# Performance work log

Hardware: AMD Instinct MI355X
Metric: run time of the kernel (lower is better)

Reference implementation:

```python
import jax, jax.numpy as jnp
import numpy as np

D_MODEL = 1024
N_HEAD = 16
D_K = D_MODEL // N_HEAD
SEQ_LEN = 2048
BATCH = 2
NEG = -1e8


def setup_inputs() -> dict:
    key = jax.random.key(0)
    ks = jax.random.split(key, 8)
    scale = 1.0 / np.sqrt(D_MODEL)
    inp = {
        "input": jax.random.normal(ks[0], (BATCH, SEQ_LEN, D_MODEL), dtype=jnp.float32),
        "mask": jax.random.randint(ks[1], (BATCH, SEQ_LEN), 0, 2) == 1,  # True = masked
        "Wq": jax.random.uniform(ks[2], (D_MODEL, D_MODEL), jnp.float32, -scale, scale),
        "bq": jax.random.uniform(ks[3], (D_MODEL,), jnp.float32, -scale, scale),
        "Wk": jax.random.uniform(ks[4], (D_MODEL, D_MODEL), jnp.float32, -scale, scale),
        "bk": jax.random.uniform(ks[5], (D_MODEL,), jnp.float32, -scale, scale),
        "Wv": jax.random.uniform(ks[6], (D_MODEL, D_MODEL), jnp.float32, -scale, scale),
        "bv": jax.random.uniform(ks[7], (D_MODEL,), jnp.float32, -scale, scale),
    }
    return inp


def reference(input, mask, Wq, bq, Wk, bk, Wv, bv):
    B, S, D = input.shape
    # nn.Linear: y = x @ W^T + b
    def split_heads(x):
        return x.reshape(B, S, N_HEAD, D_K).transpose(0, 2, 1, 3)  # [B,H,S,d_k]

    Q = split_heads(input @ Wq.T + bq)
    K = split_heads(input @ Wk.T + bk)
    V = split_heads(input @ Wv.T + bv)

    scores = jnp.einsum('bhqd,bhkd->bhqk', Q, K) / jnp.sqrt(jnp.float32(D_K))
    # mask [B,S] broadcast over heads and query positions (key mask)
    scores = jnp.where(mask[:, None, None, :], NEG, scores)
    attn = jax.nn.softmax(scores, axis=-1)
    out = jnp.einsum('bhqk,bhkd->bhqd', attn, V)  # [B,H,S,d_k]
    return out.transpose(0, 2, 1, 3).reshape(B, S, D)
```

## Files before the change

### kernel.cpp

```cpp
#include <hip/hip_runtime.h>
#include <math.h>

#define D_MODEL 1024
#define NH 16
#define DK 64
#define SEQ 2048
#define BATCH 2
#define MTOT (BATCH * SEQ)

typedef unsigned short u16;
typedef unsigned int u32;
typedef short bf16x8 __attribute__((ext_vector_type(8)));
typedef short bf16x4 __attribute__((ext_vector_type(4)));
typedef float f32x4 __attribute__((ext_vector_type(4)));

static constexpr float NEGV2 = -1e8f * 1.44269504089f;
static constexpr float SCL2  = 0.125f * 1.44269504089f;
static constexpr float MINIT = -1e30f;

__device__ __forceinline__ u16 f2bf(float f) {
    union { float f; u32 u; } v; v.f = f;
    u32 r = v.u + 0x7FFFu + ((v.u >> 16) & 1u);
    return (u16)(r >> 16);
}

__device__ __forceinline__ float fexp2(float x) {
#if __has_builtin(__builtin_amdgcn_exp2f)
    return __builtin_amdgcn_exp2f(x);
#else
    return __expf(x * 0.69314718056f);
#endif
}

__device__ __forceinline__ f32x4 mfma16(bf16x4 a, bf16x4 b, f32x4 c) {
#if __has_builtin(__builtin_amdgcn_mfma_f32_16x16x16_bf16)
    return __builtin_amdgcn_mfma_f32_16x16x16_bf16(a, b, c, 0, 0, 0);
#else
    return __builtin_amdgcn_mfma_f32_16x16x16bf16_1k(a, b, c, 0, 0, 0);
#endif
}

__device__ __forceinline__ void stage16(const u16* g, u16* lds_per_lane) {
#if __has_builtin(__builtin_amdgcn_global_load_lds)
    __builtin_amdgcn_global_load_lds((const __attribute__((address_space(1))) u32*)g,
                                     (__attribute__((address_space(3))) u32*)lds_per_lane,
                                     16, 0, 0);
#else
    *(uint4*)lds_per_lane = *(const uint4*)g;
#endif
}

__global__ __launch_bounds__(256) void convert_bf16(
    const float* __restrict__ X, const float* __restrict__ Wq,
    const float* __restrict__ Wk, const float* __restrict__ Wv,
    u16* __restrict__ Xb, u16* __restrict__ Wb)
{
    const int NX = MTOT * D_MODEL / 4;
    const int NW = D_MODEL * D_MODEL / 4;
    int i = blockIdx.x * 256 + threadIdx.x;
    if (i >= NX + 3 * NW) return;
    float4 v; u16* dst;
    if (i < NX)             { v = ((const float4*)X )[i];            dst = Xb + (size_t)i * 4; }
    else if (i < NX + NW)   { v = ((const float4*)Wq)[i - NX];       dst = Wb + (size_t)(i - NX) * 4; }
    else if (i < NX + 2*NW) { v = ((const float4*)Wk)[i - NX - NW];  dst = Wb + (size_t)NW * 4 + (size_t)(i - NX - NW) * 4; }
    else                    { v = ((const float4*)Wv)[i - NX - 2*NW];dst = Wb + (size_t)NW * 8 + (size_t)(i - NX - 2*NW) * 4; }
    ushort4 o;
    o.x = f2bf(v.x); o.y = f2bf(v.y); o.z = f2bf(v.z); o.w = f2bf(v.w);
    *(ushort4*)dst = o;
}

__global__ __launch_bounds__(256, 2) void proj_mfma(
    const u16* __restrict__ Xb, const u16* __restrict__ Wb,
    const float* __restrict__ bq, const float* __restrict__ bk, const float* __restrict__ bv,
    u16* __restrict__ Qb, u16* __restrict__ Kb, u16* __restrict__ Vb)
{
    __shared__ u16 As[128 * 32];
    __shared__ u16 Bs[128 * 32];

    const int which = blockIdx.z;
    const u16* __restrict__ W = Wb + (size_t)which * D_MODEL * D_MODEL;
    const float* __restrict__ bias = which == 0 ? bq : (which == 1 ? bk : bv);
    u16* __restrict__ Out = which == 0 ? Qb : (which == 1 ? Kb : Vb);

    const int m0 = blockIdx.x * 128, n0 = blockIdx.y * 128;
    const int tid = threadIdx.x, lane = tid & 63, w = tid >> 6;
    const int quad = lane >> 4, l15 = lane & 15;
    const int wr = w >> 1, wc = w & 1;

    f32x4 acc[4][4];
#pragma unroll
    for (int i = 0; i < 4; i++)
#pragma unroll
        for (int j = 0; j < 4; j++) acc[i][j] = (f32x4)0.0f;

    const int srow = 32 * w + (lane >> 2);
    const int scol = (lane & 3) * 8;

    for (int k0 = 0; k0 < D_MODEL; k0 += 32) {
#pragma unroll
        for (int t = 0; t < 2; t++) {
            stage16(Xb + (size_t)(m0 + srow + 16 * t) * D_MODEL + k0 + scol,
                    &As[(32 * w + 16 * t) * 32 + lane * 8]);
            stage16(W + (size_t)(n0 + srow + 16 * t) * D_MODEL + k0 + scol,
                    &Bs[(32 * w + 16 * t) * 32 + lane * 8]);
        }
        __syncthreads();
        bf16x8 af[4], bfr[4];
#pragma unroll
        for (int i = 0; i < 4; i++)
            af[i] = *(const bf16x8*)&As[(wr * 64 + i * 16 + l15) * 32 + quad * 8];
#pragma unroll
        for (int j = 0; j < 4; j++)
            bfr[j] = *(const bf16x8*)&Bs[(wc * 64 + j * 16 + l15) * 32 + quad * 8];
#pragma unroll
        for (int i = 0; i < 4; i++)
#pragma unroll
            for (int j = 0; j < 4; j++)
                acc[i][j] = __builtin_amdgcn_mfma_f32_16x16x32_bf16(af[i], bfr[j], acc[i][j], 0, 0, 0);
        __syncthreads();
    }

    float bj[4];
#pragma unroll
    for (int j = 0; j < 4; j++) bj[j] = bias[n0 + wc * 64 + j * 16 + l15];
#pragma unroll
    for (int i = 0; i < 4; i++) {
#pragma unroll
        for (int j = 0; j < 4; j++) {
#pragma unroll
            for (int r = 0; r < 4; r++) {
                int m = m0 + wr * 64 + i * 16 + quad * 4 + r;
                int n = n0 + wc * 64 + j * 16 + l15;
                int b = m >> 11, s = m & (SEQ - 1);
                int h = n >> 6, d = n & 63;
                Out[(((size_t)b * NH + h) * SEQ + s) * DK + d] = f2bf(acc[i][j][r] + bj[j]);
            }
        }
    }
}

__global__ __launch_bounds__(256, 2) void attn_mfma(
    const u16* __restrict__ Qg, const u16* __restrict__ Kg, const u16* __restrict__ Vg,
    const int* __restrict__ mask, float* __restrict__ out)
{
    constexpr int PADK = 72, PADV = 72;
    __shared__ u16 Ks[2][64 * PADK];
    __shared__ u16 Vt[2][64 * PADV];
    __shared__ float mads[SEQ];

    const int qt0 = blockIdx.x, h = blockIdx.y, b = blockIdx.z;
    const int tid = threadIdx.x, lane = tid & 63, w = tid >> 6;
    const int quad = lane >> 4, l15 = lane & 15;
    const size_t bh = (size_t)b * NH + h;
    const u16* __restrict__ Qp = Qg + (bh * SEQ + qt0 * 128) * DK;
    const u16* __restrict__ Kp = Kg + bh * SEQ * DK;
    const u16* __restrict__ Vp = Vg + bh * SEQ * DK;
    const int* __restrict__ mp = mask + b * SEQ;

    for (int i = tid; i < SEQ; i += 256) mads[i] = mp[i] ? NEGV2 : 0.0f;

    const int q0 = w * 32;
    bf16x8 qf[2][2];
#pragma unroll
    for (int qt = 0; qt < 2; qt++)
#pragma unroll
        for (int half = 0; half < 2; half++)
            qf[qt][half] = *(const bf16x8*)(Qp + (size_t)(q0 + qt * 16 + l15) * DK + half * 32 + quad * 8);

    const int skey = tid & 63, sdk = (tid >> 6) * 16;
    const int vkp2 = (tid & 31) * 2, vd0 = (tid >> 5) * 8;

    {
        const u16* kr = Kp + (size_t)skey * DK + sdk;
        bf16x8 k0 = *(const bf16x8*)kr, k1 = *(const bf16x8*)(kr + 8);
        u16* kd = &Ks[0][skey * PADK + sdk];
        *(bf16x8*)kd = k0; *(bf16x8*)(kd + 8) = k1;
        const u16* vr = Vp + (size_t)vkp2 * DK + vd0;
        bf16x8 v0 = *(const bf16x8*)vr, v1 = *(const bf16x8*)(vr + DK);
#pragma unroll
        for (int i = 0; i < 8; i++)
            *(u32*)&Vt[0][(vd0 + i) * PADV + vkp2] = (u32)(u16)v0[i] | ((u32)(u16)v1[i] << 16);
    }
    __syncthreads();

    f32x4 O[4][2];
    float mrow[2], lrow[2];
#pragma unroll
    for (int dt = 0; dt < 4; dt++)
#pragma unroll
        for (int qt = 0; qt < 2; qt++) O[dt][qt] = (f32x4)0.0f;
    mrow[0] = mrow[1] = MINIT;
    lrow[0] = lrow[1] = 0.0f;

    for (int kt = 0; kt < SEQ / 64; kt++) {
        const int bb = kt & 1;
        bf16x8 nk0, nk1, nv0, nv1;
        if (kt < SEQ / 64 - 1) {
            const u16* kr = Kp + (size_t)((kt + 1) * 64 + skey) * DK + sdk;
            nk0 = *(const bf16x8*)kr; nk1 = *(const bf16x8*)(kr + 8);
            const u16* vr = Vp + (size_t)((kt + 1) * 64 + vkp2) * DK + vd0;
            nv0 = *(const bf16x8*)vr; nv1 = *(const bf16x8*)(vr + DK);
        }

        f32x4 St[4][2];
#pragma unroll
        for (int ktl = 0; ktl < 4; ktl++) {
            bf16x8 kf0 = *(const bf16x8*)&Ks[bb][(ktl * 16 + l15) * PADK + quad * 8];
            bf16x8 kf1 = *(const bf16x8*)&Ks[bb][(ktl * 16 + l15) * PADK + 32 + quad * 8];
#pragma unroll
            for (int qt = 0; qt < 2; qt++) {
                f32x4 acc = (f32x4)0.0f;
                acc = __builtin_amdgcn_mfma_f32_16x16x32_bf16(kf0, qf[qt][0], acc, 0, 0, 0);
                acc = __builtin_amdgcn_mfma_f32_16x16x32_bf16(kf1, qf[qt][1], acc, 0, 0, 0);
                St[ktl][qt] = acc;
            }
        }

#pragma unroll
        for (int ktl = 0; ktl < 4; ktl++) {
            f32x4 ma = *(const f32x4*)&mads[kt * 64 + ktl * 16 + quad * 4];
#pragma unroll
            for (int qt = 0; qt < 2; qt++)
#pragma unroll
                for (int r = 0; r < 4; r++)
                    St[ktl][qt][r] = St[ktl][qt][r] * SCL2 + ma[r];
        }

        float alpha[2];
#pragma unroll
        for (int qt = 0; qt < 2; qt++) {
            float mx = St[0][qt][0];
#pragma unroll
            for (int ktl = 0; ktl < 4; ktl++)
#pragma unroll
                for (int r = 0; r < 4; r++) mx = fmaxf(mx, St[ktl][qt][r]);
            mx = fmaxf(mx, __shfl_xor(mx, 16));
            mx = fmaxf(mx, __shfl_xor(mx, 32));
            float mn = fmaxf(mrow[qt], mx);
            alpha[qt] = fexp2(mrow[qt] - mn);
            mrow[qt] = mn;
            float sum = 0.0f;
#pragma unroll
            for (int ktl = 0; ktl < 4; ktl++)
#pragma unroll
                for (int r = 0; r < 4; r++) {
                    float p = fexp2(St[ktl][qt][r] - mn);
                    St[ktl][qt][r] = p;
                    sum += p;
                }
            sum += __shfl_xor(sum, 16);
            sum += __shfl_xor(sum, 32);
            lrow[qt] = alpha[qt] * lrow[qt] + sum;
        }

        bf16x4 pf[4][2];
#pragma unroll
        for (int ktl = 0; ktl < 4; ktl++)
#pragma unroll
            for (int qt = 0; qt < 2; qt++) {
                bf16x4 pp;
#pragma unroll
                for (int r = 0; r < 4; r++) pp[r] = (short)f2bf(St[ktl][qt][r]);
                pf[ktl][qt] = pp;
            }

#pragma unroll
        for (int dt = 0; dt < 4; dt++)
#pragma unroll
            for (int qt = 0; qt < 2; qt++)
#pragma unroll
                for (int r = 0; r < 4; r++) O[dt][qt][r] *= alpha[qt];

#pragma unroll
        for (int ktl = 0; ktl < 4; ktl++)
#pragma unroll
            for (int dt = 0; dt < 4; dt++) {
                bf16x4 vf = *(const bf16x4*)&Vt[bb][(dt * 16 + l15) * PADV + ktl * 16 + quad * 4];
#pragma unroll
                for (int qt = 0; qt < 2; qt++)
                    O[dt][qt] = mfma16(vf, pf[ktl][qt], O[dt][qt]);
            }

        if (kt < SEQ / 64 - 1) {
            u16* kd = &Ks[bb ^ 1][skey * PADK + sdk];
            *(bf16x8*)kd = nk0; *(bf16x8*)(kd + 8) = nk1;
#pragma unroll
            for (int i = 0; i < 8; i++)
                *(u32*)&Vt[bb ^ 1][(vd0 + i) * PADV + vkp2] = (u32)(u16)nv0[i] | ((u32)(u16)nv1[i] << 16);
        }
        __syncthreads();
    }

    float inv[2] = {1.0f / lrow[0], 1.0f / lrow[1]};
#pragma unroll
    for (int qt = 0; qt < 2; qt++) {
        int q = qt0 * 128 + q0 + qt * 16 + l15;
        float* op = out + ((size_t)b * SEQ + q) * D_MODEL + h * DK;
#pragma unroll
        for (int dt = 0; dt < 4; dt++)
#pragma unroll
            for (int r = 0; r < 4; r++)
                op[dt * 16 + quad * 4 + r] = O[dt][qt][r] * inv[qt];
    }
}

extern "C" void kernel_launch(void* const* d_in, const int* in_sizes, int n_in,
                              void* d_out, int out_size, void* d_ws, size_t ws_size,
                              hipStream_t stream)
{
    const float* X  = (const float*)d_in[0];
    const int* mask = (const int*)d_in[1];
    const float* Wq = (const float*)d_in[2];
    const float* bq = (const float*)d_in[3];
    const float* Wk = (const float*)d_in[4];
    const float* bk = (const float*)d_in[5];
    const float* Wv = (const float*)d_in[6];
    const float* bv = (const float*)d_in[7];
    float* out = (float*)d_out;

    u16* Xb = (u16*)d_ws;
    u16* Wb = Xb + (size_t)MTOT * D_MODEL;
    u16* Qb = Wb + (size_t)3 * D_MODEL * D_MODEL;
    u16* Kb = Qb + (size_t)BATCH * NH * SEQ * DK;
    u16* Vb = Kb + (size_t)BATCH * NH * SEQ * DK;

    const int ncvt = (MTOT * D_MODEL + 3 * D_MODEL * D_MODEL) / 4;
    convert_bf16<<<(ncvt + 255) / 256, 256, 0, stream>>>(X, Wq, Wk, Wv, Xb, Wb);
    proj_mfma<<<dim3(MTOT / 128, D_MODEL / 128, 3), 256, 0, stream>>>(Xb, Wb, bq, bk, bv, Qb, Kb, Vb);
    attn_mfma<<<dim3(SEQ / 128, NH, BATCH), 256, 0, stream>>>(Qb, Kb, Vb, mask, out);
}
```

Measured before the change: 187.0 us.

## Split attention block into 8 waves of 16 query rows each

The attention kernel now runs 512 threads per block. Each wave owns 16 query rows instead of 32, and the cooperative K/V tile loads are split across more threads. The aim is more waves in flight to hide LDS and exp latency, and lower register pressure per thread. In exchange, each K/V fragment read from shared memory feeds half as many MFMAs, so LDS traffic per FLOP doubles, and barriers now synchronize more waves.

```diff
diff --git a/kernel.cpp b/kernel.cpp
--- a/kernel.cpp
+++ b/kernel.cpp
@@ -139,7 +139,7 @@
     }
 }
 
-__global__ __launch_bounds__(256, 2) void attn_mfma(
+__global__ __launch_bounds__(512, 4) void attn_mfma(
     const u16* __restrict__ Qg, const u16* __restrict__ Kg, const u16* __restrict__ Vg,
     const int* __restrict__ mask, float* __restrict__ out)
 {
@@ -157,150 +157,123 @@
     const u16* __restrict__ Vp = Vg + bh * SEQ * DK;
     const int* __restrict__ mp = mask + b * SEQ;
 
-    for (int i = tid; i < SEQ; i += 256) mads[i] = mp[i] ? NEGV2 : 0.0f;
-
-    const int q0 = w * 32;
-    bf16x8 qf[2][2];
-#pragma unroll
-    for (int qt = 0; qt < 2; qt++)
-#pragma unroll
-        for (int half = 0; half < 2; half++)
-            qf[qt][half] = *(const bf16x8*)(Qp + (size_t)(q0 + qt * 16 + l15) * DK + half * 32 + quad * 8);
-
-    const int skey = tid & 63, sdk = (tid >> 6) * 16;
-    const int vkp2 = (tid & 31) * 2, vd0 = (tid >> 5) * 8;
+    for (int i = tid; i < SEQ; i += 512) mads[i] = mp[i] ? NEGV2 : 0.0f;
+
+    const int q0 = w * 16;
+    bf16x8 qf[2];
+#pragma unroll
+    for (int half = 0; half < 2; half++)
+        qf[half] = *(const bf16x8*)(Qp + (size_t)(q0 + l15) * DK + half * 32 + quad * 8);
+
+    const int skey = tid & 63, sdk = (tid >> 6) * 8;
+    const int vkp2 = (tid & 31) * 2, vd0 = (tid >> 5) * 4;
 
     {
-        const u16* kr = Kp + (size_t)skey * DK + sdk;
-        bf16x8 k0 = *(const bf16x8*)kr, k1 = *(const bf16x8*)(kr + 8);
-        u16* kd = &Ks[0][skey * PADK + sdk];
-        *(bf16x8*)kd = k0; *(bf16x8*)(kd + 8) = k1;
+        *(bf16x8*)&Ks[0][skey * PADK + sdk] = *(const bf16x8*)(Kp + (size_t)skey * DK + sdk);
         const u16* vr = Vp + (size_t)vkp2 * DK + vd0;
-        bf16x8 v0 = *(const bf16x8*)vr, v1 = *(const bf16x8*)(vr + DK);
-#pragma unroll
-        for (int i = 0; i < 8; i++)
+        bf16x4 v0 = *(const bf16x4*)vr, v1 = *(const bf16x4*)(vr + DK);
+#pragma unroll
+        for (int i = 0; i < 4; i++)
             *(u32*)&Vt[0][(vd0 + i) * PADV + vkp2] = (u32)(u16)v0[i] | ((u32)(u16)v1[i] << 16);
     }
     __syncthreads();
 
-    f32x4 O[4][2];
-    float mrow[2], lrow[2];
-#pragma unroll
-    for (int dt = 0; dt < 4; dt++)
-#pragma unroll
-        for (int qt = 0; qt < 2; qt++) O[dt][qt] = (f32x4)0.0f;
-    mrow[0] = mrow[1] = MINIT;
-    lrow[0] = lrow[1] = 0.0f;
+    f32x4 O[4];
+    float mrow = MINIT, lrow = 0.0f;
+#pragma unroll
+    for (int dt = 0; dt < 4; dt++) O[dt] = (f32x4)0.0f;
 
     for (int kt = 0; kt < SEQ / 64; kt++) {
         const int bb = kt & 1;
-        bf16x8 nk0, nk1, nv0, nv1;
+        bf16x8 nk; bf16x4 nv0, nv1;
         if (kt < SEQ / 64 - 1) {
-            const u16* kr = Kp + (size_t)((kt + 1) * 64 + skey) * DK + sdk;
-            nk0 = *(const bf16x8*)kr; nk1 = *(const bf16x8*)(kr + 8);
+            nk = *(const bf16x8*)(Kp + (size_t)((kt + 1) * 64 + skey) * DK + sdk);
             const u16* vr = Vp + (size_t)((kt + 1) * 64 + vkp2) * DK + vd0;
-            nv0 = *(const bf16x8*)vr; nv1 = *(const bf16x8*)(vr + DK);
-        }
-
-        f32x4 St[4][2];
+            nv0 = *(const bf16x4*)vr; nv1 = *(const bf16x4*)(vr + DK);
+        }
+
+        f32x4 St[4];
 #pragma unroll
         for (int ktl = 0; ktl < 4; ktl++) {
             bf16x8 kf0 = *(const bf16x8*)&Ks[bb][(ktl * 16 + l15) * PADK + quad * 8];
             bf16x8 kf1 = *(const bf16x8*)&Ks[bb][(ktl * 16 + l15) * PADK + 32 + quad * 8];
-#pragma unroll
-            for (int qt = 0; qt < 2; qt++) {
-                f32x4 acc = (f32x4)0.0f;
-                acc = __builtin_amdgcn_mfma_f32_16x16x32_bf16(kf0, qf[qt][0], acc, 0, 0, 0);
-                acc = __builtin_amdgcn_mfma_f32_16x16x32_bf16(kf1, qf[qt][1], acc, 0, 0, 0);
-                St[ktl][qt] = acc;
-            }
+            f32x4 acc = (f32x4)0.0f;
+            acc = __builtin_amdgcn_mfma_f32_16x16x32_bf16(kf0, qf[0], acc, 0, 0, 0);
+            acc = __builtin_amdgcn_mfma_f32_16x16x32_bf16(kf1, qf[1], acc, 0, 0, 0);
+            St[ktl] = acc;
         }
 
 #pragma unroll
         for (int ktl = 0; ktl < 4; ktl++) {
             f32x4 ma = *(const f32x4*)&mads[kt * 64 + ktl * 16 + quad * 4];
 #pragma unroll
-            for (int qt = 0; qt < 2; qt++)
-#pragma unroll
-                for (int r = 0; r < 4; r++)
-                    St[ktl][qt][r] = St[ktl][qt][r] * SCL2 + ma[r];
-        }
-
-        float alpha[2];
-#pragma unroll
-        for (int qt = 0; qt < 2; qt++) {
-            float mx = St[0][qt][0];
-#pragma unroll
-            for (int ktl = 0; ktl < 4; ktl++)
-#pragma unroll
-                for (int r = 0; r < 4; r++) mx = fmaxf(mx, St[ktl][qt][r]);
-            mx = fmaxf(mx, __shfl_xor(mx, 16));
-            mx = fmaxf(mx, __shfl_xor(mx, 32));
-            float mn = fmaxf(mrow[qt], mx);
-            alpha[qt] = fexp2(mrow[qt] - mn);
-            mrow[qt] = mn;
-            float sum = 0.0f;
-#pragma unroll
-            for (int ktl = 0; ktl < 4; ktl++)
-#pragma unroll
-                for (int r = 0; r < 4; r++) {
-                    float p = fexp2(St[ktl][qt][r] - mn);
-                    St[ktl][qt][r] = p;
-                    sum += p;
-                }
-            sum += __shfl_xor(sum, 16);
-            sum += __shfl_xor(sum, 32);
-            lrow[qt] = alpha[qt] * lrow[qt] + sum;
-        }
-
-        bf16x4 pf[4][2];
+            for (int r = 0; r < 4; r++)
+                St[ktl][r] = St[ktl][r] * SCL2 + ma[r];
+        }
+
+        float mx = St[0][0];
 #pragma unroll
         for (int ktl = 0; ktl < 4; ktl++)
 #pragma unroll
-            for (int qt = 0; qt < 2; qt++) {
-                bf16x4 pp;
-#pragma unroll
-                for (int r = 0; r < 4; r++) pp[r] = (short)f2bf(St[ktl][qt][r]);
-                pf[ktl][qt] = pp;
+            for (int r = 0; r < 4; r++) mx = fmaxf(mx, St[ktl][r]);
+        mx = fmaxf(mx, __shfl_xor(mx, 16));
+        mx = fmaxf(mx, __shfl_xor(mx, 32));
+        float mn = fmaxf(mrow, mx);
+        float alpha = fexp2(mrow - mn);
+        mrow = mn;
+        float sum = 0.0f;
+#pragma unroll
+        for (int ktl = 0; ktl < 4; ktl++)
+#pragma unroll
+            for (int r = 0; r < 4; r++) {
+                float p = fexp2(St[ktl][r] - mn);
+                St[ktl][r] = p;
+                sum += p;
             }
+        sum += __shfl_xor(sum, 16);
+        sum += __shfl_xor(sum, 32);
+        lrow = alpha * lrow + sum;
+
+        bf16x4 pf[4];
+#pragma unroll
+        for (int ktl = 0; ktl < 4; ktl++) {
+            bf16x4 pp;
+#pragma unroll
+            for (int r = 0; r < 4; r++) pp[r] = (short)f2bf(St[ktl][r]);
+            pf[ktl] = pp;
+        }
 
 #pragma unroll
         for (int dt = 0; dt < 4; dt++)
 #pragma unroll
-            for (int qt = 0; qt < 2; qt++)
-#pragma unroll
-                for (int r = 0; r < 4; r++) O[dt][qt][r] *= alpha[qt];
+            for (int r = 0; r < 4; r++) O[dt][r] *= alpha;
 
 #pragma unroll
         for (int ktl = 0; ktl < 4; ktl++)
 #pragma unroll
             for (int dt = 0; dt < 4; dt++) {
                 bf16x4 vf = *(const bf16x4*)&Vt[bb][(dt * 16 + l15) * PADV + ktl * 16 + quad * 4];
-#pragma unroll
-                for (int qt = 0; qt < 2; qt++)
-                    O[dt][qt] = mfma16(vf, pf[ktl][qt], O[dt][qt]);
+                O[dt] = mfma16(vf, pf[ktl], O[dt]);
             }
 
         if (kt < SEQ / 64 - 1) {
-            u16* kd = &Ks[bb ^ 1][skey * PADK + sdk];
-            *(bf16x8*)kd = nk0; *(bf16x8*)(kd + 8) = nk1;
-#pragma unroll
-            for (int i = 0; i < 8; i++)
+            *(bf16x8*)&Ks[bb ^ 1][skey * PADK + sdk] = nk;
+#pragma unroll
+            for (int i = 0; i < 4; i++)
                 *(u32*)&Vt[bb ^ 1][(vd0 + i) * PADV + vkp2] = (u32)(u16)nv0[i] | ((u32)(u16)nv1[i] << 16);
         }
         __syncthreads();
     }
 
-    float inv[2] = {1.0f / lrow[0], 1.0f / lrow[1]};
-#pragma unroll
-    for (int qt = 0; qt < 2; qt++) {
-        int q = qt0 * 128 + q0 + qt * 16 + l15;
+    float inv = 1.0f / lrow;
+    {
+        int q = qt0 * 128 + q0 + l15;
         float* op = out + ((size_t)b * SEQ + q) * D_MODEL + h * DK;
 #pragma unroll
         for (int dt = 0; dt < 4; dt++)
 #pragma unroll
             for (int r = 0; r < 4; r++)
-                op[dt * 16 + quad * 4 + r] = O[dt][qt][r] * inv[qt];
+                op[dt * 16 + quad * 4 + r] = O[dt][r] * inv;
     }
 }
 
@@ -327,5 +300,5 @@
     const int ncvt = (MTOT * D_MODEL + 3 * D_MODEL * D_MODEL) / 4;
     convert_bf16<<<(ncvt + 255) / 256, 256, 0, stream>>>(X, Wq, Wk, Wv, Xb, Wb);
     proj_mfma<<<dim3(MTOT / 128, D_MODEL / 128, 3), 256, 0, stream>>>(Xb, Wb, bq, bk, bv, Qb, Kb, Vb);
-    attn_mfma<<<dim3(SEQ / 128, NH, BATCH), 256, 0, stream>>>(Qb, Kb, Vb, mask, out);
-}
+    attn_mfma<<<dim3(SEQ / 128, NH, BATCH), 512, 0, stream>>>(Qb, Kb, Vb, mask, out);
+}
```

Result: slower. 193.0 us (+3.2%).
